# Kernel optimization log

Measured on AMD Instinct MI355X. Metric: run time of the kernel, lower is better.

The kernel has to match this reference:

```python
import jax, jax.numpy as jnp
import numpy as np

B, F, E = 2048, 24, 128
P = F * (F - 1) // 2  # 276 upper-triangular field pairs


def setup_inputs() -> dict:
    key = jax.random.key(0)
    k1, k2 = jax.random.split(key)
    x = jax.random.normal(k1, (B, F, E), dtype=jnp.float32)
    # keras random_normal initializer uses small stddev; 0.05 mirrors that
    kernel = jax.random.normal(k2, (E, P, E), dtype=jnp.float32) * 0.05
    return {"x": x, "kernel": kernel}


def reference(x, kernel):
    F_ = x.shape[1]
    p_idx, q_idx = np.triu_indices(F_, k=1)  # static pair index lists (i < j)
    Xp = x[:, p_idx, :]  # [B, P, E]
    Xq = x[:, q_idx, :]  # [B, P, E]
    # result[b,p] = sum_{d,e} Xp[b,p,e] * kernel[d,p,e] * Xq[b,p,d]
    # fused einsum avoids the [B, E, P, E] intermediate the TF code materializes
    result = jnp.einsum("bpe,dpe,bpd->bp", Xp, kernel, Xq)
    return result
```

## Files before the change

kernel.cpp:

```cpp
#include <hip/hip_runtime.h>
#include <stdint.h>

#define B_SZ 2048
#define F_SZ 24
#define E_SZ 128
#define P_SZ 276
#define NWG  552

#define XT_ELEMS (B_SZ * F_SZ * E_SZ)
#define WS_NEED  ((size_t)XT_ELEMS * 2)

#define XPREP_BLKS (F_SZ * 64)

typedef __bf16 bf16x8 __attribute__((ext_vector_type(8)));
typedef __bf16 bf16x4 __attribute__((ext_vector_type(4)));
typedef float  f32x16 __attribute__((ext_vector_type(16)));

__global__ __launch_bounds__(256) void prepack_x(
    const float* __restrict__ x, __bf16* __restrict__ xft)
{
    const int bid = blockIdx.x;
    const int tid = threadIdx.x;
    const int f = bid >> 6, grp = bid & 63;
    __shared__ float sT[32][129];
    {
        const int row = tid >> 3, c0 = (tid & 7) * 16;
        const float* src = x + ((size_t)(grp * 32 + row) * F_SZ + f) * E_SZ + c0;
        float4 v0 = ((const float4*)src)[0];
        float4 v1 = ((const float4*)src)[1];
        float4 v2 = ((const float4*)src)[2];
        float4 v3 = ((const float4*)src)[3];
        *(float4*)&sT[row][c0]      = v0;
        *(float4*)&sT[row][c0 + 4]  = v1;
        *(float4*)&sT[row][c0 + 8]  = v2;
        *(float4*)&sT[row][c0 + 12] = v3;
    }
    __syncthreads();
    __bf16* dst = xft + (size_t)(f * 64 + grp) * 4096;
#pragma unroll
    for (int u = 0; u < 2; ++u) {
        const int s = tid * 2 + u;
        const int row = s & 31;
        const int e0  = (s >> 6) * 16 + ((s >> 5) & 1) * 8;
        bf16x8 h;
#pragma unroll
        for (int i = 0; i < 8; ++i)
            h[i] = (__bf16)sT[row][e0 + i];
        *(bf16x8*)(dst + s * 8) = h;
    }
}

__global__ __launch_bounds__(512, 4) void opn_main(
    const __bf16* __restrict__ xft, const float* __restrict__ kern,
    float* __restrict__ out)
{
    __shared__ short sK[E_SZ * E_SZ];

    const int tid = threadIdx.x, w = tid >> 6, lane = tid & 63;
    const int l31 = lane & 31, hi = lane >> 5;
    const int orig = blockIdx.x;
    const int xcd = orig & 7;
    const int p = ((xcd >> 1) * 69) + (orig >> 3);
    const int h = xcd & 1;

    int fp = 0, rem = p;
    while (rem >= F_SZ - 1 - fp) { rem -= F_SZ - 1 - fp; ++fp; }
    const int fq = fp + 1 + rem;

    {
        const int d = tid >> 2, c = tid & 3;
        const float* kr = kern + ((size_t)d * P_SZ + p) * E_SZ + c * 32;
        float4 v[8];
#pragma unroll
        for (int j = 0; j < 8; ++j) v[j] = ((const float4*)kr)[j];
        const int dsw = d & 15;
#pragma unroll
        for (int j = 0; j < 4; ++j) {
            bf16x8 hh;
            hh[0] = (__bf16)v[2*j].x;   hh[1] = (__bf16)v[2*j].y;
            hh[2] = (__bf16)v[2*j].z;   hh[3] = (__bf16)v[2*j].w;
            hh[4] = (__bf16)v[2*j+1].x; hh[5] = (__bf16)v[2*j+1].y;
            hh[6] = (__bf16)v[2*j+1].z; hh[7] = (__bf16)v[2*j+1].w;
            const int s = c * 4 + j;
            *(bf16x8*)&sK[d * E_SZ + ((s ^ dsw) << 3)] = hh;
        }
    }
    __syncthreads();

#pragma unroll
    for (int t = 0; t < 4; ++t) {
        const int grp = h * 32 + t * 8 + w;

        bf16x8 xpf[8];
        const __bf16* xpb = xft + (size_t)(fp * 64 + grp) * 4096 + lane * 8;
#pragma unroll
        for (int kk = 0; kk < 8; ++kk)
            xpf[kk] = *(const bf16x8*)(xpb + kk * 512);

        bf16x4 xqr[4][4];
        const __bf16* xqb = xft + (size_t)(fq * 64 + grp) * 4096 + l31 * 8 + hi * 4;
#pragma unroll
        for (int mt = 0; mt < 4; ++mt)
#pragma unroll
            for (int q = 0; q < 4; ++q)
                xqr[mt][q] = *(const bf16x4*)(xqb + (mt * 2 + (q >> 1)) * 512 + (q & 1) * 256);

        float s0 = 0.f, s1 = 0.f;
#pragma unroll
        for (int mt = 0; mt < 4; ++mt) {
            const int arow = mt * 32 + l31;
            const short* kRow = &sK[arow * E_SZ];
            const int asw = (arow & 15) << 3;
            f32x16 acc;
#pragma unroll
            for (int q = 0; q < 16; ++q) acc[q] = 0.f;
#pragma unroll
            for (int kk = 0; kk < 8; ++kk) {
                bf16x8 afr = *(const bf16x8*)&kRow[((kk * 2 + hi) << 3) ^ asw];
                acc = __builtin_amdgcn_mfma_f32_32x32x16_bf16(afr, xpf[kk], acc, 0, 0, 0);
            }
#pragma unroll
            for (int q = 0; q < 4; ++q) {
                const bf16x4 xq = xqr[mt][q];
                s0 += acc[q * 4 + 0] * (float)xq[0] + acc[q * 4 + 1] * (float)xq[1];
                s1 += acc[q * 4 + 2] * (float)xq[2] + acc[q * 4 + 3] * (float)xq[3];
            }
        }
        float s = s0 + s1;
        s += __shfl_xor(s, 32);
        if (hi == 0)
            out[(size_t)(grp * 32 + l31) * P_SZ + p] = s;
    }
}

__global__ __launch_bounds__(512, 4) void opn_fallback(
    const float* __restrict__ x, const float* __restrict__ kern,
    float* __restrict__ out)
{
    __shared__ short sA[128 * E_SZ];
    __shared__ short sB[E_SZ * E_SZ];
    __shared__ float red[2][128];

    const int tid = threadIdx.x;
    const int orig = blockIdx.x;
    const int nwg2 = P_SZ * 16;
    const int wgid = (orig & 7) * (nwg2 / 8) + (orig >> 3);
    const int p  = wgid >> 4;
    const int bb = wgid & 15;
    const int b0 = bb * 128;

    int fp = 0, rem = p;
    while (rem >= F_SZ - 1 - fp) { rem -= F_SZ - 1 - fp; ++fp; }
    const int fq = fp + 1 + rem;

#pragma unroll
    for (int k = 0; k < 4; ++k) {
        int i = tid + k * 512;
        int r = i >> 4, s8 = i & 15;
        const float* src = x + ((size_t)(b0 + r) * F_SZ + fp) * E_SZ + s8 * 8;
        float4 v0 = *(const float4*)src;
        float4 v1 = *(const float4*)(src + 4);
        bf16x8 hh;
        hh[0] = (__bf16)v0.x; hh[1] = (__bf16)v0.y; hh[2] = (__bf16)v0.z; hh[3] = (__bf16)v0.w;
        hh[4] = (__bf16)v1.x; hh[5] = (__bf16)v1.y; hh[6] = (__bf16)v1.z; hh[7] = (__bf16)v1.w;
        *(bf16x8*)&sA[r * E_SZ + ((s8 ^ (r & 15)) << 3)] = hh;
    }
#pragma unroll
    for (int k = 0; k < 4; ++k) {
        int i = tid + k * 512;
        int r = i >> 4, s8 = i & 15;
        const float* src = kern + ((size_t)r * P_SZ + p) * E_SZ + s8 * 8;
        float4 v0 = *(const float4*)src;
        float4 v1 = *(const float4*)(src + 4);
        bf16x8 hh;
        hh[0] = (__bf16)v0.x; hh[1] = (__bf16)v0.y; hh[2] = (__bf16)v0.z; hh[3] = (__bf16)v0.w;
        hh[4] = (__bf16)v1.x; hh[5] = (__bf16)v1.y; hh[6] = (__bf16)v1.z; hh[7] = (__bf16)v1.w;
        *(bf16x8*)&sB[r * E_SZ + ((s8 ^ (r & 15)) << 3)] = hh;
    }
    __syncthreads();

    const int w = tid >> 6, lane = tid & 63;
    const int l31 = lane & 31, hi = lane >> 5;
    const int mh = w >> 2, ng = w & 3;

    f32x16 acc[2];
#pragma unroll
    for (int mt = 0; mt < 2; ++mt)
#pragma unroll
        for (int j = 0; j < 16; ++j) acc[mt][j] = 0.f;

    const int brow = ng * 32 + l31;
#pragma unroll
    for (int kk = 0; kk < 8; ++kk) {
        const int e8 = kk * 2 + hi;
        bf16x8 bfr = *(const bf16x8*)&sA[brow * E_SZ + ((e8 ^ (brow & 15)) << 3)];
#pragma unroll
        for (int mt = 0; mt < 2; ++mt) {
            int arow = (mh * 2 + mt) * 32 + l31;
            bf16x8 afr = *(const bf16x8*)&sB[arow * E_SZ + ((e8 ^ (arow & 15)) << 3)];
            acc[mt] = __builtin_amdgcn_mfma_f32_32x32x16_bf16(afr, bfr, acc[mt], 0, 0, 0);
        }
    }

    const float* xqp = x + ((size_t)(b0 + brow) * F_SZ + fq) * E_SZ;
    float sv = 0.f;
#pragma unroll
    for (int mt = 0; mt < 2; ++mt) {
        const int dbase = (mh * 2 + mt) * 32 + hi * 4;
#pragma unroll
        for (int q = 0; q < 4; ++q) {
            float4 xq = *(const float4*)(xqp + dbase + q * 8);
            sv += acc[mt][q * 4 + 0] * xq.x + acc[mt][q * 4 + 1] * xq.y
                + acc[mt][q * 4 + 2] * xq.z + acc[mt][q * 4 + 3] * xq.w;
        }
    }
    sv += __shfl_xor(sv, 32);
    if (hi == 0) red[mh][brow] = sv;
    __syncthreads();

    if (tid < 128)
        out[(size_t)(b0 + tid) * P_SZ + p] = red[0][tid] + red[1][tid];
}

extern "C" void kernel_launch(void* const* d_in, const int* in_sizes, int n_in,
                              void* d_out, int out_size, void* d_ws, size_t ws_size,
                              hipStream_t stream) {
    const float* x    = (const float*)d_in[0];
    const float* kern = (const float*)d_in[1];
    float* out = (float*)d_out;

    if (ws_size >= WS_NEED) {
        __bf16* xft = (__bf16*)d_ws;
        prepack_x<<<dim3(XPREP_BLKS), 256, 0, stream>>>(x, xft);
        opn_main<<<dim3(NWG), 512, 0, stream>>>(xft, kern, out);
    } else {
        opn_fallback<<<dim3(P_SZ * 16), 512, 0, stream>>>(x, kern, out);
    }
}
```

Measured before the change: 50.30 us.

## Split batch across four workgroups per pair and hoist kernel fragments to registers

Doubles the grid to four workgroups per field pair, each handling a quarter of the batch with two iterations instead of four. The first X tile loads are issued before the kernel slice is staged to LDS, so global X traffic overlaps the kernel conversion. The whole per-lane kernel fragment set (32 bf16x8 vectors) is loaded from LDS once into registers and reused across iterations. In exchange, each kernel slice is read and converted four times instead of twice, register pressure rises sharply under the 512x4 launch bound with possible spills, and the XCD-aware block mapping is dropped.

```diff
diff --git a/kernel.cpp b/kernel.cpp
--- a/kernel.cpp
+++ b/kernel.cpp
@@ -5,7 +5,7 @@
 #define F_SZ 24
 #define E_SZ 128
 #define P_SZ 276
-#define NWG  552
+#define NWG  (P_SZ * 4)
 
 #define XT_ELEMS (B_SZ * F_SZ * E_SZ)
 #define WS_NEED  ((size_t)XT_ELEMS * 2)
@@ -59,13 +59,28 @@
     const int tid = threadIdx.x, w = tid >> 6, lane = tid & 63;
     const int l31 = lane & 31, hi = lane >> 5;
     const int orig = blockIdx.x;
-    const int xcd = orig & 7;
-    const int p = ((xcd >> 1) * 69) + (orig >> 3);
-    const int h = xcd & 1;
+    const int bb2 = orig & 3;
+    const int p   = orig >> 2;
 
     int fp = 0, rem = p;
     while (rem >= F_SZ - 1 - fp) { rem -= F_SZ - 1 - fp; ++fp; }
     const int fq = fp + 1 + rem;
+
+    bf16x8 xpf[8];
+    bf16x4 xqr[4][4];
+    {
+        const int grp = bb2 * 16 + w;
+        const __bf16* xpb = xft + (size_t)(fp * 64 + grp) * 4096 + lane * 8;
+#pragma unroll
+        for (int kk = 0; kk < 8; ++kk)
+            xpf[kk] = *(const bf16x8*)(xpb + kk * 512);
+        const __bf16* xqb = xft + (size_t)(fq * 64 + grp) * 4096 + l31 * 8 + hi * 4;
+#pragma unroll
+        for (int mt = 0; mt < 4; ++mt)
+#pragma unroll
+            for (int q = 0; q < 4; ++q)
+                xqr[mt][q] = *(const bf16x4*)(xqb + (mt * 2 + (q >> 1)) * 512 + (q & 1) * 256);
+    }
 
     {
         const int d = tid >> 2, c = tid & 3;
@@ -87,38 +102,42 @@
     }
     __syncthreads();
 
-#pragma unroll
-    for (int t = 0; t < 4; ++t) {
-        const int grp = h * 32 + t * 8 + w;
-
-        bf16x8 xpf[8];
-        const __bf16* xpb = xft + (size_t)(fp * 64 + grp) * 4096 + lane * 8;
+    bf16x8 kf[4][8];
+#pragma unroll
+    for (int mt = 0; mt < 4; ++mt) {
+        const int arow = mt * 32 + l31;
+        const short* kRow = &sK[arow * E_SZ];
+        const int asw = (arow & 15) << 3;
 #pragma unroll
         for (int kk = 0; kk < 8; ++kk)
-            xpf[kk] = *(const bf16x8*)(xpb + kk * 512);
-
-        bf16x4 xqr[4][4];
-        const __bf16* xqb = xft + (size_t)(fq * 64 + grp) * 4096 + l31 * 8 + hi * 4;
-#pragma unroll
-        for (int mt = 0; mt < 4; ++mt)
-#pragma unroll
-            for (int q = 0; q < 4; ++q)
-                xqr[mt][q] = *(const bf16x4*)(xqb + (mt * 2 + (q >> 1)) * 512 + (q & 1) * 256);
+            kf[mt][kk] = *(const bf16x8*)&kRow[((kk * 2 + hi) << 3) ^ asw];
+    }
+
+#pragma unroll
+    for (int t = 0; t < 2; ++t) {
+        const int grp = bb2 * 16 + t * 8 + w;
+        if (t > 0) {
+            const __bf16* xpb = xft + (size_t)(fp * 64 + grp) * 4096 + lane * 8;
+#pragma unroll
+            for (int kk = 0; kk < 8; ++kk)
+                xpf[kk] = *(const bf16x8*)(xpb + kk * 512);
+            const __bf16* xqb = xft + (size_t)(fq * 64 + grp) * 4096 + l31 * 8 + hi * 4;
+#pragma unroll
+            for (int mt = 0; mt < 4; ++mt)
+#pragma unroll
+                for (int q = 0; q < 4; ++q)
+                    xqr[mt][q] = *(const bf16x4*)(xqb + (mt * 2 + (q >> 1)) * 512 + (q & 1) * 256);
+        }
 
         float s0 = 0.f, s1 = 0.f;
 #pragma unroll
         for (int mt = 0; mt < 4; ++mt) {
-            const int arow = mt * 32 + l31;
-            const short* kRow = &sK[arow * E_SZ];
-            const int asw = (arow & 15) << 3;
             f32x16 acc;
 #pragma unroll
             for (int q = 0; q < 16; ++q) acc[q] = 0.f;
 #pragma unroll
-            for (int kk = 0; kk < 8; ++kk) {
-                bf16x8 afr = *(const bf16x8*)&kRow[((kk * 2 + hi) << 3) ^ asw];
-                acc = __builtin_amdgcn_mfma_f32_32x32x16_bf16(afr, xpf[kk], acc, 0, 0, 0);
-            }
+            for (int kk = 0; kk < 8; ++kk)
+                acc = __builtin_amdgcn_mfma_f32_32x32x16_bf16(kf[mt][kk], xpf[kk], acc, 0, 0, 0);
 #pragma unroll
             for (int q = 0; q < 4; ++q) {
                 const bf16x4 xq = xqr[mt][q];
```

Result: slower. 114.9 us (+128.4%).
